# Performance work log

Measured on AMD Instinct MI355X. Metric: run time of the kernel, lower is better.

The kernel has to match this reference:

```python
import jax, jax.numpy as jnp
import numpy as np

C, P, G = 80, 30000, 800       # classes, preds/class, gts/class
IOU_THR = 0.5
IMG = 1024.0                   # synthetic image size
BATCH = 16                     # images per batch (box[0] = image index)


def _make_boxes(key, n_cls, n):
    """Boxes in the module's 7-col layout: [img_idx, class, score, x1, y1, x2, y2]."""
    k1, k2, k3, k4 = jax.random.split(key, 4)
    xy = jax.random.uniform(k1, (n_cls, n, 2), minval=0.0, maxval=IMG - 128.0)
    wh = jax.random.uniform(k2, (n_cls, n, 2), minval=4.0, maxval=128.0)
    score = jax.random.uniform(k3, (n_cls, n, 1))
    img_idx = jax.random.randint(k4, (n_cls, n, 1), 0, BATCH).astype(jnp.float32)
    cls = jnp.zeros((n_cls, n, 1), jnp.float32)
    return jnp.concatenate([img_idx, cls, score, xy, xy + wh], axis=-1)


def setup_inputs() -> dict:
    key = jax.random.key(0)
    kp, kg = jax.random.split(key)
    return {"pred_boxes": _make_boxes(kp, C, P), "gt_boxes": _make_boxes(kg, C, G)}


def _pairwise_iou(a, b):
    # a: [P,4], b: [G,4] corner-format xyxy -> [P,G]
    lt = jnp.maximum(a[:, None, :2], b[None, :, :2])
    rb = jnp.minimum(a[:, None, 2:], b[None, :, 2:])
    wh = jnp.clip(rb - lt, 0.0)
    inter = wh[..., 0] * wh[..., 1]
    area_a = (a[:, 2] - a[:, 0]) * (a[:, 3] - a[:, 1])
    area_b = (b[:, 2] - b[:, 0]) * (b[:, 3] - b[:, 1])
    return inter / (area_a[:, None] + area_b[None, :] - inter + 1e-9)


def _ap_one_class(pb, gb):
    # pb: [P,7] preds, gb: [G,7] gts for one class
    n_p, n_g = pb.shape[0], gb.shape[0]
    order = jnp.argsort(-pb[:, 2])             # sort preds by score desc
    boxes = pb[order, 3:7]
    iou = _pairwise_iou(boxes, gb[:, 3:7])     # [P,G]
    best_iou = iou.max(axis=1)
    match = iou.argmax(axis=1)                 # best gt per pred
    valid = best_iou > IOU_THR
    p_idx = jnp.arange(n_p, dtype=jnp.int32)
    # first (highest-score) valid pred claiming each gt -> TP; later claims -> FP
    first = jnp.full((n_g,), n_p, jnp.int32).at[match].min(
        jnp.where(valid, p_idx, n_p))
    tp = (valid & (p_idx == first[match])).astype(jnp.float32)
    ctp = jnp.cumsum(tp)
    cfp = jnp.cumsum(1.0 - tp)
    recall = ctp / (n_g + 1e-9)
    precision = ctp / (ctp + cfp + 1e-9)
    # trapezoidal AP over the PR curve (torch.trapz(precisions, recalls))
    return jnp.sum((recall[1:] - recall[:-1]) * (precision[1:] + precision[:-1]) * 0.5)


def reference(pred_boxes, gt_boxes):
    # sequential map over classes keeps peak memory at one [P,G] IoU matrix
    aps = jax.lax.map(lambda ab: _ap_one_class(ab[0], ab[1]), (pred_boxes, gt_boxes))
    return jnp.mean(aps)
```

## Files before the change

kernel.cpp:

```cpp
#include <hip/hip_runtime.h>

#define C 80
#define P 30000
#define G 800
#define BS 256
#define NB 16
#define NC (NB * NB)
#define PPT 2
#define HCH 8
#define CHSZ ((P + HCH - 1) / HCH)


__device__ __forceinline__ unsigned long long pack_key(float s, int p) {
    return ((unsigned long long)__float_as_uint(s) << 32) | (unsigned)(P - 1 - p);
}

__global__ __launch_bounds__(BS) void gt_bin_kernel(
        const float* __restrict__ gt,
        unsigned short* __restrict__ gtCnt, unsigned short* __restrict__ gtOff,
        float4* __restrict__ gtBox, float* __restrict__ gtAbe,
        unsigned short* __restrict__ gtIdx,
        unsigned long long* __restrict__ gtKey, int* __restrict__ gHist) {
    __shared__ int h[NC], cur[NC];
    __shared__ int gcell[G];
    const int c = blockIdx.x, tid = threadIdx.x;
    h[tid] = 0;
    for (int i = tid; i < G; i += BS) gtKey[c * G + i] = 0ull;
    for (int j = tid; j < 1024; j += BS) gHist[c * 1024 + j] = 0;
    __syncthreads();
    for (int i = tid; i < G; i += BS) {
        const float* r = gt + ((size_t)c * G + i) * 7;
        float cxf = 0.5f * (r[3] + r[5]), cyf = 0.5f * (r[4] + r[6]);
        int bx = min(max((int)(cxf * (1.0f / 64.0f)), 0), NB - 1);
        int by = min(max((int)(cyf * (1.0f / 64.0f)), 0), NB - 1);
        int cl = by * NB + bx;
        gcell[i] = cl;
        atomicAdd(&h[cl], 1);
    }
    __syncthreads();
    const int v = h[tid];
    cur[tid] = v;
    __syncthreads();
    for (int o = 1; o < NC; o <<= 1) {
        int t = (tid >= o) ? cur[tid - o] : 0;
        __syncthreads();
        cur[tid] += t;
        __syncthreads();
    }
    const int excl = cur[tid] - v;
    gtOff[c * NC + tid] = (unsigned short)excl;
    gtCnt[c * NC + tid] = (unsigned short)v;
    __syncthreads();
    cur[tid] = excl;
    __syncthreads();
    for (int i = tid; i < G; i += BS) {
        const float* r = gt + ((size_t)c * G + i) * 7;
        float x1 = r[3], y1 = r[4], x2 = r[5], y2 = r[6];
        int slot = atomicAdd(&cur[gcell[i]], 1);
        gtBox[c * G + slot] = make_float4(x1, y1, x2, y2);
        gtAbe[c * G + slot] = __fadd_rn(__fmul_rn(__fsub_rn(x2, x1), __fsub_rn(y2, y1)), 1e-9f);
        gtIdx[c * G + slot] = (unsigned short)i;
    }
}

__global__ __launch_bounds__(BS) void match3_kernel(
        const float* __restrict__ pred,
        const unsigned short* __restrict__ gtOff, const unsigned short* __restrict__ gtCnt,
        const float4* __restrict__ gtBox, const float* __restrict__ gtAbe,
        const unsigned short* __restrict__ gtIdx,
        float* __restrict__ scoreC,
        unsigned long long* __restrict__ gtKey) {
    __shared__ float sX1[G], sY1[G], sX2[G], sY2[G], sE[G];
    __shared__ unsigned short sG[G];
    __shared__ unsigned short sOff[NC], sCnt[NC];
    const int c = blockIdx.y, tid = threadIdx.x;

    for (int i = tid; i < G; i += BS) {
        float4 b = gtBox[c * G + i];
        sX1[i] = b.x; sY1[i] = b.y; sX2[i] = b.z; sY2[i] = b.w;
        sE[i] = gtAbe[c * G + i];
        sG[i] = gtIdx[c * G + i];
    }
    sOff[tid] = gtOff[c * NC + tid];
    sCnt[tid] = gtCnt[c * NC + tid];
    __syncthreads();

    const size_t cp = (size_t)c * P;
    #pragma unroll
    for (int rep = 0; rep < PPT; ++rep) {
        const int p = (blockIdx.x * PPT + rep) * BS + tid;
        if (p < P) {
            const float* r = pred + (cp + p) * 7;
            float s   = r[2];
            float ax1 = r[3], ay1 = r[4], ax2 = r[5], ay2 = r[6];
            scoreC[cp + p] = s;
            float A = __fmul_rn(__fsub_rn(ax2, ax1), __fsub_rn(ay2, ay1));
            float cxf = 0.5f * (ax1 + ax2), cyf = 0.5f * (ay1 + ay2);
            int cx = min(max((int)(cxf * (1.0f / 64.0f)), 0), NB - 1);
            int cy = min(max((int)(cyf * (1.0f / 64.0f)), 0), NB - 1);
            int x0 = max(cx - 1, 0), x1 = min(cx + 1, NB - 1);
            int y0 = max(cy - 1, 0), y1 = min(cy + 1, NB - 1);
            float IN = 0.0f, SB = 1.0f;
            int mj = -1;
            for (int yy = y0; yy <= y1; ++yy) {
                const int rowb = yy * NB;
                const int jb = sOff[rowb + x0];
                const int je = sOff[rowb + x1] + sCnt[rowb + x1];
                for (int j = jb; j < je; ++j) {
                    float bx1 = sX1[j], by1 = sY1[j];
                    float bx2 = sX2[j], by2 = sY2[j];
                    float lx = fmaxf(ax1, bx1), ly = fmaxf(ay1, by1);
                    float rx = fminf(ax2, bx2), ry = fminf(ay2, by2);
                    float wx = fmaxf(__fsub_rn(rx, lx), 0.0f);
                    float wy = fmaxf(__fsub_rn(ry, ly), 0.0f);
                    float in = __fmul_rn(wx, wy);
                    float sb = __fadd_rn(A, sE[j]);
                    bool  up = __fmul_rn(in, SB) > __fmul_rn(IN, sb);
                    IN = up ? in : IN; SB = up ? sb : SB; mj = up ? j : mj;
                }
            }
            if (IN > 0.0f) {
                float bx1 = sX1[mj], by1 = sY1[mj], bx2 = sX2[mj], by2 = sY2[mj];
                float area = __fmul_rn(__fsub_rn(bx2, bx1), __fsub_rn(by2, by1));
                float dn = __fadd_rn(__fsub_rn(__fadd_rn(A, area), IN), 1e-9f);
                float iou = __fdiv_rn(IN, dn);
                if (iou > 0.5f)
                    atomicMax(&gtKey[c * G + sG[mj]], pack_key(s, p));
            }
        }
    }
}

__global__ __launch_bounds__(BS) void sortc_kernel(
        const unsigned long long* __restrict__ gtKey,
        unsigned long long* __restrict__ sortedKeys, int* __restrict__ sortT) {
    __shared__ unsigned long long k[G];
    __shared__ unsigned long long sk[1024];
    __shared__ int cnt;
    const int c = blockIdx.x, tid = threadIdx.x;
    if (tid == 0) cnt = 0;
    for (int j = tid; j < 1024; j += BS) sk[j] = 0ull;
    __syncthreads();
    for (int i = tid; i < G; i += BS) {
        unsigned long long key = gtKey[c * G + i];
        if (key != 0ull) k[atomicAdd(&cnt, 1)] = key;
    }
    __syncthreads();
    const int T = cnt;
    if (tid == 0) sortT[c] = T;
    for (int t = tid; t < T; t += BS) {
        unsigned long long key = k[t];
        int pos = 0;
        for (int u = 0; u < T; ++u) pos += (k[u] > key) ? 1 : 0;
        sk[pos] = key;
    }
    __syncthreads();
    for (int j = tid; j < 1024; j += BS) sortedKeys[c * 1024 + j] = sk[j];
}

__global__ __launch_bounds__(BS) void hist_kernel(
        const float* __restrict__ scoreC,
        const unsigned long long* __restrict__ sortedKeys,
        int* __restrict__ gHist) {
    __shared__ unsigned long long sK[1024];
    __shared__ int h[1024];
    const int c = blockIdx.y, tid = threadIdx.x;
    for (int j = tid; j < 1024; j += BS) { sK[j] = sortedKeys[c * 1024 + j]; h[j] = 0; }
    __syncthreads();
    const int start = blockIdx.x * CHSZ;
    const int end   = min(start + CHSZ, P);
    const float* sc = scoreC + (size_t)c * P;
    for (int i = start + tid; i < end; i += BS) {
        unsigned long long kq =
            ((unsigned long long)__float_as_uint(sc[i]) << 32) | (unsigned)(P - 1 - i);
        int lo = 0;
        #pragma unroll
        for (int step = 512; step > 0; step >>= 1)
            if (sK[lo + step - 1] > kq) lo += step;
        atomicAdd(&h[lo], 1);
    }
    __syncthreads();
    for (int j = tid; j < 1024; j += BS)
        if (h[j]) atomicAdd(&gHist[c * 1024 + j], h[j]);
}

__global__ __launch_bounds__(BS) void ap2_kernel(
        const int* __restrict__ sortT, const int* __restrict__ gHist,
        float* __restrict__ ap) {
    __shared__ int ha[1024];
    __shared__ int hb[1024];
    __shared__ float red[BS];
    const int c = blockIdx.x, tid = threadIdx.x;
    const int T = sortT[c];
    for (int j = tid; j < 1024; j += BS) ha[j] = gHist[c * 1024 + j];
    __syncthreads();
    int* src = ha; int* dst = hb;
    for (int o = 1; o < 1024; o <<= 1) {
        for (int j = tid; j < 1024; j += BS)
            dst[j] = src[j] + ((j >= o) ? src[j - o] : 0);
        __syncthreads();
        int* tmp = src; src = dst; dst = tmp;
    }
    float sum = 0.0f;
    for (int s = tid; s < T; s += BS) {
        int r = src[s] - 1;
        if (r >= 1) {
            float kf  = (float)(s + 1);
            float km  = (float)s;
            float ri  = __fdiv_rn(kf, 800.0f);
            float rim = __fdiv_rn(km, 800.0f);
            float pi  = __fdiv_rn(kf, (float)(r + 1));
            float pim = __fdiv_rn(km, (float)r);
            sum = __fadd_rn(sum,
                  __fmul_rn(__fmul_rn(__fsub_rn(ri, rim), __fadd_rn(pi, pim)), 0.5f));
        }
    }
    red[tid] = sum;
    __syncthreads();
    for (int s2 = BS / 2; s2 > 0; s2 >>= 1) {
        if (tid < s2) red[tid] = __fadd_rn(red[tid], red[tid + s2]);
        __syncthreads();
    }
    if (tid == 0) ap[c] = red[0];
}

__global__ void mean_kernel(const float* __restrict__ ap, float* __restrict__ out) {
    if (threadIdx.x == 0) {
        float s = 0.0f;
        for (int c = 0; c < C; ++c) s = __fadd_rn(s, ap[c]);
        out[0] = __fdiv_rn(s, 80.0f);
    }
}

extern "C" void kernel_launch(void* const* d_in, const int* in_sizes, int n_in,
                              void* d_out, int out_size, void* d_ws, size_t ws_size,
                              hipStream_t stream) {
    const float* pred = (const float*)d_in[0];
    const float* gt   = (const float*)d_in[1];
    float* out = (float*)d_out;

    char* ws = (char*)d_ws;
    int*                sortT      = (int*)               (ws + 0);
    float*              ap         = (float*)             (ws + 512);
    unsigned short*     gtCnt      = (unsigned short*)    (ws + 1024);
    unsigned short*     gtOff      = (unsigned short*)    (ws + 41984);
    unsigned short*     gtIdx      = (unsigned short*)    (ws + 82944);
    float*              gtAbe      = (float*)             (ws + 210944);
    float4*             gtBox      = (float4*)            (ws + 466944);
    unsigned long long* gtKey      = (unsigned long long*)(ws + 1490944);
    unsigned long long* sortedKeys = (unsigned long long*)(ws + 2002944);
    int*                gHist      = (int*)               (ws + 2658304);
    float*              scoreC     = (float*)             (ws + 2985984);

    const int M_BLK = (P + BS * PPT - 1) / (BS * PPT);

    gt_bin_kernel<<<C, BS, 0, stream>>>(gt, gtCnt, gtOff, gtBox, gtAbe, gtIdx, gtKey, gHist);
    match3_kernel<<<dim3(M_BLK, C), BS, 0, stream>>>(pred, gtOff, gtCnt, gtBox, gtAbe, gtIdx,
                                                     scoreC, gtKey);
    sortc_kernel<<<C, BS, 0, stream>>>(gtKey, sortedKeys, sortT);
    hist_kernel<<<dim3(HCH, C), BS, 0, stream>>>(scoreC, sortedKeys, gHist);
    ap2_kernel<<<C, BS, 0, stream>>>(sortT, gHist, ap);
    mean_kernel<<<1, 64, 0, stream>>>(ap, out);
}
```

Before: 243.2 us.

## Bin predictions by spatial cell before matching to cut wave divergence

Adds three passes: a per-cell prediction histogram, a prefix scan, and a scatter that reorders prediction boxes by grid cell. The matcher then walks the reordered boxes, so lanes in a wave search neighbouring cells with similar GT loop lengths instead of random ones. Scatter and match run in chunks of 20 classes to bound the scratch buffer. The cost is two extra full reads of the prediction array, an extra indirection for score and index on matches, and more kernel launches.

```diff
diff --git a/kernel.cpp b/kernel.cpp
--- a/kernel.cpp
+++ b/kernel.cpp
@@ -7,12 +7,20 @@
 #define NB 16
 #define NC (NB * NB)
 #define PPT 2
+#define CH 20
+#define NCHK (C / CH)
 #define HCH 8
 #define CHSZ ((P + HCH - 1) / HCH)
 
 
 __device__ __forceinline__ unsigned long long pack_key(float s, int p) {
     return ((unsigned long long)__float_as_uint(s) << 32) | (unsigned)(P - 1 - p);
+}
+
+__device__ __forceinline__ int cell_of_center(float cxf, float cyf) {
+    int bx = min(max((int)(cxf * (1.0f / 64.0f)), 0), NB - 1);
+    int by = min(max((int)(cyf * (1.0f / 64.0f)), 0), NB - 1);
+    return by * NB + bx;
 }
 
 __global__ __launch_bounds__(BS) void gt_bin_kernel(
@@ -20,20 +28,19 @@
         unsigned short* __restrict__ gtCnt, unsigned short* __restrict__ gtOff,
         float4* __restrict__ gtBox, float* __restrict__ gtAbe,
         unsigned short* __restrict__ gtIdx,
-        unsigned long long* __restrict__ gtKey, int* __restrict__ gHist) {
+        unsigned long long* __restrict__ gtKey, int* __restrict__ gHist,
+        int* __restrict__ predCnt) {
     __shared__ int h[NC], cur[NC];
     __shared__ int gcell[G];
     const int c = blockIdx.x, tid = threadIdx.x;
     h[tid] = 0;
+    predCnt[c * NC + tid] = 0;
     for (int i = tid; i < G; i += BS) gtKey[c * G + i] = 0ull;
     for (int j = tid; j < 1024; j += BS) gHist[c * 1024 + j] = 0;
     __syncthreads();
     for (int i = tid; i < G; i += BS) {
         const float* r = gt + ((size_t)c * G + i) * 7;
-        float cxf = 0.5f * (r[3] + r[5]), cyf = 0.5f * (r[4] + r[6]);
-        int bx = min(max((int)(cxf * (1.0f / 64.0f)), 0), NB - 1);
-        int by = min(max((int)(cyf * (1.0f / 64.0f)), 0), NB - 1);
-        int cl = by * NB + bx;
+        int cl = cell_of_center(0.5f * (r[3] + r[5]), 0.5f * (r[4] + r[6]));
         gcell[i] = cl;
         atomicAdd(&h[cl], 1);
     }
@@ -63,17 +70,81 @@
     }
 }
 
-__global__ __launch_bounds__(BS) void match3_kernel(
-        const float* __restrict__ pred,
+__global__ __launch_bounds__(BS) void pred_prep_kernel(
+        const float* __restrict__ pred, int* __restrict__ predCnt,
+        float* __restrict__ scoreC) {
+    __shared__ int h[NC];
+    const int c = blockIdx.y, tid = threadIdx.x;
+    h[tid] = 0;
+    __syncthreads();
+    int p = blockIdx.x * BS + tid;
+    if (p < P) {
+        const float* r = pred + ((size_t)c * P + p) * 7;
+        scoreC[(size_t)c * P + p] = r[2];
+        int cl = cell_of_center(0.5f * (r[3] + r[5]), 0.5f * (r[4] + r[6]));
+        atomicAdd(&h[cl], 1);
+    }
+    __syncthreads();
+    if (h[tid]) atomicAdd(&predCnt[c * NC + tid], h[tid]);
+}
+
+__global__ __launch_bounds__(NC) void pred_scan_kernel(
+        const int* __restrict__ predCnt,
+        unsigned short* __restrict__ predOff, int* __restrict__ predCur) {
+    __shared__ int sc[NC];
+    const int c = blockIdx.x, tid = threadIdx.x;
+    const int v = predCnt[c * NC + tid];
+    sc[tid] = v;
+    __syncthreads();
+    for (int o = 1; o < NC; o <<= 1) {
+        int t = (tid >= o) ? sc[tid - o] : 0;
+        __syncthreads();
+        sc[tid] += t;
+        __syncthreads();
+    }
+    const int excl = sc[tid] - v;
+    predOff[c * NC + tid] = (unsigned short)excl;
+    predCur[c * NC + tid] = excl;
+}
+
+__global__ __launch_bounds__(BS) void pred_scatter_kernel(
+        const float* __restrict__ pred, int* __restrict__ predCur,
+        float4* __restrict__ predSorted, unsigned short* __restrict__ pIdxS,
+        int c0) {
+    __shared__ int h[NC], base[NC];
+    const int cl_loc = blockIdx.y, c = c0 + cl_loc, tid = threadIdx.x;
+    h[tid] = 0;
+    __syncthreads();
+    int p = blockIdx.x * BS + tid;
+    int cellv = 0, lr = 0;
+    float4 box = make_float4(0.f, 0.f, 0.f, 0.f);
+    if (p < P) {
+        const float* r = pred + ((size_t)c * P + p) * 7;
+        box = make_float4(r[3], r[4], r[5], r[6]);
+        cellv = cell_of_center(0.5f * (box.x + box.z), 0.5f * (box.y + box.w));
+        lr = atomicAdd(&h[cellv], 1);
+    }
+    __syncthreads();
+    if (h[tid]) base[tid] = atomicAdd(&predCur[c * NC + tid], h[tid]);
+    __syncthreads();
+    if (p < P) {
+        int slot = base[cellv] + lr;
+        predSorted[(size_t)cl_loc * P + slot] = box;
+        pIdxS[(size_t)cl_loc * P + slot] = (unsigned short)p;
+    }
+}
+
+__global__ __launch_bounds__(BS) void match5_kernel(
+        const float4* __restrict__ predSorted, const unsigned short* __restrict__ pIdxS,
         const unsigned short* __restrict__ gtOff, const unsigned short* __restrict__ gtCnt,
         const float4* __restrict__ gtBox, const float* __restrict__ gtAbe,
         const unsigned short* __restrict__ gtIdx,
-        float* __restrict__ scoreC,
-        unsigned long long* __restrict__ gtKey) {
+        const float* __restrict__ scoreC,
+        unsigned long long* __restrict__ gtKey, int c0) {
     __shared__ float sX1[G], sY1[G], sX2[G], sY2[G], sE[G];
     __shared__ unsigned short sG[G];
     __shared__ unsigned short sOff[NC], sCnt[NC];
-    const int c = blockIdx.y, tid = threadIdx.x;
+    const int cl_loc = blockIdx.y, c = c0 + cl_loc, tid = threadIdx.x;
 
     for (int i = tid; i < G; i += BS) {
         float4 b = gtBox[c * G + i];
@@ -85,19 +156,16 @@
     sCnt[tid] = gtCnt[c * NC + tid];
     __syncthreads();
 
-    const size_t cp = (size_t)c * P;
+    const size_t cpl = (size_t)cl_loc * P;
     #pragma unroll
     for (int rep = 0; rep < PPT; ++rep) {
-        const int p = (blockIdx.x * PPT + rep) * BS + tid;
-        if (p < P) {
-            const float* r = pred + (cp + p) * 7;
-            float s   = r[2];
-            float ax1 = r[3], ay1 = r[4], ax2 = r[5], ay2 = r[6];
-            scoreC[cp + p] = s;
+        const int s = (blockIdx.x * PPT + rep) * BS + tid;
+        if (s < P) {
+            float4 b4 = predSorted[cpl + s];
+            float ax1 = b4.x, ay1 = b4.y, ax2 = b4.z, ay2 = b4.w;
             float A = __fmul_rn(__fsub_rn(ax2, ax1), __fsub_rn(ay2, ay1));
-            float cxf = 0.5f * (ax1 + ax2), cyf = 0.5f * (ay1 + ay2);
-            int cx = min(max((int)(cxf * (1.0f / 64.0f)), 0), NB - 1);
-            int cy = min(max((int)(cyf * (1.0f / 64.0f)), 0), NB - 1);
+            int cell = cell_of_center(0.5f * (ax1 + ax2), 0.5f * (ay1 + ay2));
+            int cx = cell & (NB - 1), cy = cell >> 4;
             int x0 = max(cx - 1, 0), x1 = min(cx + 1, NB - 1);
             int y0 = max(cy - 1, 0), y1 = min(cy + 1, NB - 1);
             float IN = 0.0f, SB = 1.0f;
@@ -124,8 +192,11 @@
                 float area = __fmul_rn(__fsub_rn(bx2, bx1), __fsub_rn(by2, by1));
                 float dn = __fadd_rn(__fsub_rn(__fadd_rn(A, area), IN), 1e-9f);
                 float iou = __fdiv_rn(IN, dn);
-                if (iou > 0.5f)
-                    atomicMax(&gtKey[c * G + sG[mj]], pack_key(s, p));
+                if (iou > 0.5f) {
+                    int p = pIdxS[cpl + s];
+                    float sscore = scoreC[(size_t)c * P + p];
+                    atomicMax(&gtKey[c * G + sG[mj]], pack_key(sscore, p));
+                }
             }
         }
     }
@@ -242,21 +313,36 @@
     char* ws = (char*)d_ws;
     int*                sortT      = (int*)               (ws + 0);
     float*              ap         = (float*)             (ws + 512);
-    unsigned short*     gtCnt      = (unsigned short*)    (ws + 1024);
-    unsigned short*     gtOff      = (unsigned short*)    (ws + 41984);
-    unsigned short*     gtIdx      = (unsigned short*)    (ws + 82944);
-    float*              gtAbe      = (float*)             (ws + 210944);
-    float4*             gtBox      = (float4*)            (ws + 466944);
-    unsigned long long* gtKey      = (unsigned long long*)(ws + 1490944);
-    unsigned long long* sortedKeys = (unsigned long long*)(ws + 2002944);
-    int*                gHist      = (int*)               (ws + 2658304);
-    float*              scoreC     = (float*)             (ws + 2985984);
-
+    int*                predCnt    = (int*)               (ws + 1024);
+    unsigned short*     predOff    = (unsigned short*)    (ws + 82944);
+    unsigned short*     gtCnt      = (unsigned short*)    (ws + 123904);
+    unsigned short*     gtOff      = (unsigned short*)    (ws + 164864);
+    unsigned short*     gtIdx      = (unsigned short*)    (ws + 205824);
+    unsigned short*     pIdxS      = (unsigned short*)    (ws + 333824);
+    float*              gtAbe      = (float*)             (ws + 1533824);
+    float4*             gtBox      = (float4*)            (ws + 1789824);
+    unsigned long long* gtKey      = (unsigned long long*)(ws + 2813824);
+    unsigned long long* sortedKeys = (unsigned long long*)(ws + 3325824);
+    int*                predCur    = (int*)               (ws + 3325824);
+    int*                gHist      = (int*)               (ws + 3981184);
+    float*              scoreC     = (float*)             (ws + 4308864);
+    float4*             predSorted = (float4*)            (ws + 13908864);
+
+    const int P_BLK = (P + BS - 1) / BS;
     const int M_BLK = (P + BS * PPT - 1) / (BS * PPT);
 
-    gt_bin_kernel<<<C, BS, 0, stream>>>(gt, gtCnt, gtOff, gtBox, gtAbe, gtIdx, gtKey, gHist);
-    match3_kernel<<<dim3(M_BLK, C), BS, 0, stream>>>(pred, gtOff, gtCnt, gtBox, gtAbe, gtIdx,
-                                                     scoreC, gtKey);
+    gt_bin_kernel<<<C, BS, 0, stream>>>(gt, gtCnt, gtOff, gtBox, gtAbe, gtIdx,
+                                        gtKey, gHist, predCnt);
+    pred_prep_kernel<<<dim3(P_BLK, C), BS, 0, stream>>>(pred, predCnt, scoreC);
+    pred_scan_kernel<<<C, NC, 0, stream>>>(predCnt, predOff, predCur);
+    for (int k = 0; k < NCHK; ++k) {
+        const int c0 = k * CH;
+        pred_scatter_kernel<<<dim3(P_BLK, CH), BS, 0, stream>>>(pred, predCur,
+                                                                predSorted, pIdxS, c0);
+        match5_kernel<<<dim3(M_BLK, CH), BS, 0, stream>>>(predSorted, pIdxS,
+                                                          gtOff, gtCnt, gtBox, gtAbe, gtIdx,
+                                                          scoreC, gtKey, c0);
+    }
     sortc_kernel<<<C, BS, 0, stream>>>(gtKey, sortedKeys, sortT);
     hist_kernel<<<dim3(HCH, C), BS, 0, stream>>>(scoreC, sortedKeys, gHist);
     ap2_kernel<<<C, BS, 0, stream>>>(sortT, gHist, ap);
```

Result: slower. 304.4 us (+25.1%).

## Sort predictions by grid cell in-block, drop score buffer, fuse mean into AP

Applied to the files above, without the earlier changes.

The match kernel now gives each block 2048 predictions. It bins them by spatial cell with a shared-memory counting sort, so threads in a wavefront scan the same GT neighbourhoods. This is meant to cut branch divergence from uneven loop trip counts. The separate score buffer is dropped, so the hist kernel reads scores straight from the strided pred array. The final mean kernel is folded into the AP kernel through a last-block atomic counter. The cost is fewer match blocks (15×80) with extra sort and sync overhead, plus strided score reads in hist.

```diff
diff --git a/kernel.cpp b/kernel.cpp
--- a/kernel.cpp
+++ b/kernel.cpp
@@ -6,13 +6,20 @@
 #define BS 256
 #define NB 16
 #define NC (NB * NB)
-#define PPT 2
+#define PPT 8
+#define TPB (BS * PPT)
 #define HCH 8
 #define CHSZ ((P + HCH - 1) / HCH)
 
 
 __device__ __forceinline__ unsigned long long pack_key(float s, int p) {
     return ((unsigned long long)__float_as_uint(s) << 32) | (unsigned)(P - 1 - p);
+}
+
+__device__ __forceinline__ int cell_of_center(float cxf, float cyf) {
+    int bx = min(max((int)(cxf * (1.0f / 64.0f)), 0), NB - 1);
+    int by = min(max((int)(cyf * (1.0f / 64.0f)), 0), NB - 1);
+    return by * NB + bx;
 }
 
 __global__ __launch_bounds__(BS) void gt_bin_kernel(
@@ -20,20 +27,19 @@
         unsigned short* __restrict__ gtCnt, unsigned short* __restrict__ gtOff,
         float4* __restrict__ gtBox, float* __restrict__ gtAbe,
         unsigned short* __restrict__ gtIdx,
-        unsigned long long* __restrict__ gtKey, int* __restrict__ gHist) {
+        unsigned long long* __restrict__ gtKey, int* __restrict__ gHist,
+        unsigned int* __restrict__ doneCnt) {
     __shared__ int h[NC], cur[NC];
     __shared__ int gcell[G];
     const int c = blockIdx.x, tid = threadIdx.x;
     h[tid] = 0;
+    if (c == 0 && tid == 0) *doneCnt = 0u;
     for (int i = tid; i < G; i += BS) gtKey[c * G + i] = 0ull;
     for (int j = tid; j < 1024; j += BS) gHist[c * 1024 + j] = 0;
     __syncthreads();
     for (int i = tid; i < G; i += BS) {
         const float* r = gt + ((size_t)c * G + i) * 7;
-        float cxf = 0.5f * (r[3] + r[5]), cyf = 0.5f * (r[4] + r[6]);
-        int bx = min(max((int)(cxf * (1.0f / 64.0f)), 0), NB - 1);
-        int by = min(max((int)(cyf * (1.0f / 64.0f)), 0), NB - 1);
-        int cl = by * NB + bx;
+        int cl = cell_of_center(0.5f * (r[3] + r[5]), 0.5f * (r[4] + r[6]));
         gcell[i] = cl;
         atomicAdd(&h[cl], 1);
     }
@@ -63,17 +69,21 @@
     }
 }
 
-__global__ __launch_bounds__(BS) void match3_kernel(
+__global__ __launch_bounds__(BS) void match6_kernel(
         const float* __restrict__ pred,
         const unsigned short* __restrict__ gtOff, const unsigned short* __restrict__ gtCnt,
         const float4* __restrict__ gtBox, const float* __restrict__ gtAbe,
         const unsigned short* __restrict__ gtIdx,
-        float* __restrict__ scoreC,
         unsigned long long* __restrict__ gtKey) {
     __shared__ float sX1[G], sY1[G], sX2[G], sY2[G], sE[G];
     __shared__ unsigned short sG[G];
     __shared__ unsigned short sOff[NC], sCnt[NC];
+    __shared__ unsigned char  sCell[TPB];
+    __shared__ unsigned short sIdx[TPB];
+    __shared__ int hcnt[NC], bb[NC];
     const int c = blockIdx.y, tid = threadIdx.x;
+    const int p0 = blockIdx.x * TPB;
+    const int cntP = min(TPB, P - p0);
 
     for (int i = tid; i < G; i += BS) {
         float4 b = gtBox[c * G + i];
@@ -83,23 +93,60 @@
     }
     sOff[tid] = gtOff[c * NC + tid];
     sCnt[tid] = gtCnt[c * NC + tid];
+    hcnt[tid] = 0;
     __syncthreads();
 
     const size_t cp = (size_t)c * P;
+
+    unsigned char  cellA[PPT];
+    unsigned short lrA[PPT];
     #pragma unroll
     for (int rep = 0; rep < PPT; ++rep) {
-        const int p = (blockIdx.x * PPT + rep) * BS + tid;
+        const int li = rep * BS + tid;
+        const int p  = p0 + li;
+        int cell = 0, lr = 0;
         if (p < P) {
             const float* r = pred + (cp + p) * 7;
-            float s   = r[2];
+            cell = cell_of_center(0.5f * (r[3] + r[5]), 0.5f * (r[4] + r[6]));
+            lr = atomicAdd(&hcnt[cell], 1);
+        }
+        sCell[li] = (unsigned char)cell;
+        cellA[rep] = (unsigned char)cell;
+        lrA[rep] = (unsigned short)lr;
+    }
+    __syncthreads();
+
+    const int v = hcnt[tid];
+    __syncthreads();
+    for (int o = 1; o < NC; o <<= 1) {
+        int t = (tid >= o) ? hcnt[tid - o] : 0;
+        __syncthreads();
+        hcnt[tid] += t;
+        __syncthreads();
+    }
+    bb[tid] = hcnt[tid] - v;
+    __syncthreads();
+
+    #pragma unroll
+    for (int rep = 0; rep < PPT; ++rep) {
+        const int li = rep * BS + tid;
+        if (p0 + li < P) sIdx[bb[cellA[rep]] + lrA[rep]] = (unsigned short)li;
+    }
+    __syncthreads();
+
+    #pragma unroll 1
+    for (int rep = 0; rep < PPT; ++rep) {
+        const int si = rep * BS + tid;
+        if (si < cntP) {
+            const int li = sIdx[si];
+            const int p  = p0 + li;
+            const float* r = pred + (cp + p) * 7;
             float ax1 = r[3], ay1 = r[4], ax2 = r[5], ay2 = r[6];
-            scoreC[cp + p] = s;
             float A = __fmul_rn(__fsub_rn(ax2, ax1), __fsub_rn(ay2, ay1));
-            float cxf = 0.5f * (ax1 + ax2), cyf = 0.5f * (ay1 + ay2);
-            int cx = min(max((int)(cxf * (1.0f / 64.0f)), 0), NB - 1);
-            int cy = min(max((int)(cyf * (1.0f / 64.0f)), 0), NB - 1);
-            int x0 = max(cx - 1, 0), x1 = min(cx + 1, NB - 1);
-            int y0 = max(cy - 1, 0), y1 = min(cy + 1, NB - 1);
+            const int cell = sCell[li];
+            const int cx = cell & (NB - 1), cy = cell >> 4;
+            const int x0 = max(cx - 1, 0), x1 = min(cx + 1, NB - 1);
+            const int y0 = max(cy - 1, 0), y1 = min(cy + 1, NB - 1);
             float IN = 0.0f, SB = 1.0f;
             int mj = -1;
             for (int yy = y0; yy <= y1; ++yy) {
@@ -124,8 +171,10 @@
                 float area = __fmul_rn(__fsub_rn(bx2, bx1), __fsub_rn(by2, by1));
                 float dn = __fadd_rn(__fsub_rn(__fadd_rn(A, area), IN), 1e-9f);
                 float iou = __fdiv_rn(IN, dn);
-                if (iou > 0.5f)
-                    atomicMax(&gtKey[c * G + sG[mj]], pack_key(s, p));
+                if (iou > 0.5f) {
+                    float sscore = r[2];
+                    atomicMax(&gtKey[c * G + sG[mj]], pack_key(sscore, p));
+                }
             }
         }
     }
@@ -159,7 +208,7 @@
 }
 
 __global__ __launch_bounds__(BS) void hist_kernel(
-        const float* __restrict__ scoreC,
+        const float* __restrict__ pred,
         const unsigned long long* __restrict__ sortedKeys,
         int* __restrict__ gHist) {
     __shared__ unsigned long long sK[1024];
@@ -169,10 +218,11 @@
     __syncthreads();
     const int start = blockIdx.x * CHSZ;
     const int end   = min(start + CHSZ, P);
-    const float* sc = scoreC + (size_t)c * P;
+    const float* pr = pred + (size_t)c * P * 7;
     for (int i = start + tid; i < end; i += BS) {
         unsigned long long kq =
-            ((unsigned long long)__float_as_uint(sc[i]) << 32) | (unsigned)(P - 1 - i);
+            ((unsigned long long)__float_as_uint(pr[(size_t)i * 7 + 2]) << 32)
+            | (unsigned)(P - 1 - i);
         int lo = 0;
         #pragma unroll
         for (int step = 512; step > 0; step >>= 1)
@@ -184,9 +234,10 @@
         if (h[j]) atomicAdd(&gHist[c * 1024 + j], h[j]);
 }
 
-__global__ __launch_bounds__(BS) void ap2_kernel(
+__global__ __launch_bounds__(BS) void ap2m_kernel(
         const int* __restrict__ sortT, const int* __restrict__ gHist,
-        float* __restrict__ ap) {
+        float* __restrict__ ap, unsigned int* __restrict__ doneCnt,
+        float* __restrict__ out) {
     __shared__ int ha[1024];
     __shared__ int hb[1024];
     __shared__ float red[BS];
@@ -221,14 +272,16 @@
         if (tid < s2) red[tid] = __fadd_rn(red[tid], red[tid + s2]);
         __syncthreads();
     }
-    if (tid == 0) ap[c] = red[0];
-}
-
-__global__ void mean_kernel(const float* __restrict__ ap, float* __restrict__ out) {
-    if (threadIdx.x == 0) {
-        float s = 0.0f;
-        for (int c = 0; c < C; ++c) s = __fadd_rn(s, ap[c]);
-        out[0] = __fdiv_rn(s, 80.0f);
+    if (tid == 0) {
+        ap[c] = red[0];
+        __threadfence();
+        unsigned int t = atomicAdd(doneCnt, 1u);
+        if (t == C - 1) {
+            __threadfence();
+            float s = 0.0f;
+            for (int c2 = 0; c2 < C; ++c2) s = __fadd_rn(s, ap[c2]);
+            out[0] = __fdiv_rn(s, 80.0f);
+        }
     }
 }
 
@@ -242,6 +295,7 @@
     char* ws = (char*)d_ws;
     int*                sortT      = (int*)               (ws + 0);
     float*              ap         = (float*)             (ws + 512);
+    unsigned int*       doneCnt    = (unsigned int*)      (ws + 896);
     unsigned short*     gtCnt      = (unsigned short*)    (ws + 1024);
     unsigned short*     gtOff      = (unsigned short*)    (ws + 41984);
     unsigned short*     gtIdx      = (unsigned short*)    (ws + 82944);
@@ -250,15 +304,14 @@
     unsigned long long* gtKey      = (unsigned long long*)(ws + 1490944);
     unsigned long long* sortedKeys = (unsigned long long*)(ws + 2002944);
     int*                gHist      = (int*)               (ws + 2658304);
-    float*              scoreC     = (float*)             (ws + 2985984);
-
-    const int M_BLK = (P + BS * PPT - 1) / (BS * PPT);
-
-    gt_bin_kernel<<<C, BS, 0, stream>>>(gt, gtCnt, gtOff, gtBox, gtAbe, gtIdx, gtKey, gHist);
-    match3_kernel<<<dim3(M_BLK, C), BS, 0, stream>>>(pred, gtOff, gtCnt, gtBox, gtAbe, gtIdx,
-                                                     scoreC, gtKey);
+
+    const int M_BLK = (P + TPB - 1) / TPB;
+
+    gt_bin_kernel<<<C, BS, 0, stream>>>(gt, gtCnt, gtOff, gtBox, gtAbe, gtIdx,
+                                        gtKey, gHist, doneCnt);
+    match6_kernel<<<dim3(M_BLK, C), BS, 0, stream>>>(pred, gtOff, gtCnt, gtBox,
+                                                     gtAbe, gtIdx, gtKey);
     sortc_kernel<<<C, BS, 0, stream>>>(gtKey, sortedKeys, sortT);
-    hist_kernel<<<dim3(HCH, C), BS, 0, stream>>>(scoreC, sortedKeys, gHist);
-    ap2_kernel<<<C, BS, 0, stream>>>(sortT, gHist, ap);
-    mean_kernel<<<1, 64, 0, stream>>>(ap, out);
-}
+    hist_kernel<<<dim3(HCH, C), BS, 0, stream>>>(pred, sortedKeys, gHist);
+    ap2m_kernel<<<C, BS, 0, stream>>>(sortT, gHist, ap, doneCnt, out);
+}
```

Measured after the change: 230.5 us. 5.2% less time.
